# Kernel tuning notes

Hardware: AMD Instinct MI355X
Metric: run time of the kernel (lower is better)

Reference implementation:

```python
import jax, jax.numpy as jnp
import numpy as np

N = 100000   # nodes
E = 800000   # edges (avg degree 8)
D = 64       # in_feats == n_hidden
L = 3        # n_layers
BN_EPS = 1e-5


def _l2norm(h):
    # F.normalize(dim=-1), eps=1e-12
    n = jnp.linalg.norm(h, axis=-1, keepdims=True)
    return h / jnp.maximum(n, 1e-12)


def setup_inputs() -> dict:
    key = jax.random.key(0)
    ks = jax.random.split(key, 16)
    s = 0.05
    x = jax.random.uniform(ks[0], (N, D), dtype=jnp.float32) * 10.0  # count-like, nonneg
    edge_src = jax.random.randint(ks[1], (E,), 0, N, dtype=jnp.int32)
    edge_dst = jax.random.randint(ks[2], (E,), 0, N, dtype=jnp.int32)
    return {
        "x": x,
        "edge_src": edge_src,
        "edge_dst": edge_dst,
        "W_self": jax.random.normal(ks[3], (L, D, D), jnp.float32) * s,
        "W_neigh": jax.random.normal(ks[4], (L, D, D), jnp.float32) * s,
        "b_sage": jnp.zeros((L, D), jnp.float32),
        "fc_w": jax.random.normal(ks[5], (D, D), jnp.float32) * s,
        "fc_b": jnp.zeros((D,), jnp.float32),
        "bn_gamma": jnp.ones((D,), jnp.float32),
        "bn_beta": jnp.zeros((D,), jnp.float32),
        "bn_mean": jax.random.normal(ks[6], (D,), jnp.float32) * 0.1,
        "bn_var": jax.random.uniform(ks[7], (D,), jnp.float32) + 0.5,
        "fc21_w": jax.random.normal(ks[8], (D, D), jnp.float32) * s,
        "fc21_b": jnp.zeros((D,), jnp.float32),
        "fc22_w": jax.random.normal(ks[9], (D, D), jnp.float32) * s,
        "fc22_b": jnp.zeros((D,), jnp.float32),
    }


def reference(x, edge_src, edge_dst, W_self, W_neigh, b_sage, fc_w, fc_b,
              bn_gamma, bn_beta, bn_mean, bn_var, fc21_w, fc21_b, fc22_w, fc22_b):
    n = x.shape[0]
    h = jnp.log(x + 1.0)
    # mean-aggregator degree normalization (clamped at 1 like DGL)
    deg = jax.ops.segment_sum(jnp.ones(edge_dst.shape, h.dtype), edge_dst, num_segments=n)
    deg = jnp.maximum(deg, 1.0)[:, None]
    for l in range(L):
        neigh = jax.ops.segment_sum(h[edge_src], edge_dst, num_segments=n) / deg
        h = h @ W_self[l] + neigh @ W_neigh[l] + b_sage[l]
        if l < L - 1:  # last SAGEConv has no activation / norm
            h = _l2norm(jax.nn.relu(h))
    # fc head: Linear -> BatchNorm1d(eval) -> ReLU -> Softplus
    h = h @ fc_w + fc_b
    h = (h - bn_mean) * jax.lax.rsqrt(bn_var + BN_EPS) * bn_gamma + bn_beta
    h = jax.nn.relu(h)
    h = jax.nn.softplus(h)
    z_loc = h @ fc21_w + fc21_b
    z_scale = jnp.exp(h @ fc22_w + fc22_b)
    return (z_loc, z_scale)
```

## Files before the change

### kernel.cpp

```cpp
#include <hip/hip_runtime.h>
#include <math.h>

#define NN 100000
#define NE 800000
#define NB 512
#define EPB 4096

typedef short bf16x8 __attribute__((ext_vector_type(8)));
typedef float f32x4 __attribute__((ext_vector_type(4)));
typedef unsigned short u16x8 __attribute__((ext_vector_type(8)));
typedef unsigned short u16x4 __attribute__((ext_vector_type(4)));

__device__ __forceinline__ float bf2f(unsigned short u) {
    union { unsigned u32; float f; } c; c.u32 = ((unsigned)u) << 16; return c.f;
}
__device__ __forceinline__ unsigned short f2bf(float f) {
    union { float f; unsigned u; } c; c.f = f;
    unsigned u = c.u;
    unsigned r = (u + 0x7fffu + ((u >> 16) & 1u)) >> 16;
    return (unsigned short)r;
}
__device__ __forceinline__ int bucket_of(int d) {
    return (int)(((long long)d * NB) / NN);
}
__device__ __forceinline__ int node_start_of(int b) {
    return (int)(((long long)b * NN) / NB);
}


__global__ void zero_kernel(int* __restrict__ deg, int* __restrict__ gcursor) {
    int i = blockIdx.x * 256 + threadIdx.x;
    if (i < NN) deg[i] = 0;
    if (i < NB) gcursor[i] = 0;
}

__global__ void deg_kernel(const int* __restrict__ dst, int* __restrict__ deg) {
    int e = blockIdx.x * 256 + threadIdx.x;
    if (e < NE) atomicAdd(&deg[dst[e]], 1);
}

__global__ void partial_sum_kernel(const int* __restrict__ deg, int* __restrict__ partial) {
    int base = blockIdx.x * 2048 + threadIdx.x * 8;
    int s = 0;
    #pragma unroll
    for (int j = 0; j < 8; j++) { int i = base + j; if (i < NN) s += deg[i]; }
    #pragma unroll
    for (int off = 32; off > 0; off >>= 1) s += __shfl_down(s, off);
    __shared__ int ws[4];
    int lane = threadIdx.x & 63, w = threadIdx.x >> 6;
    if (lane == 0) ws[w] = s;
    __syncthreads();
    if (threadIdx.x == 0) partial[blockIdx.x] = ws[0] + ws[1] + ws[2] + ws[3];
}

__global__ void scan_partials_kernel(int* __restrict__ partial) {
    int lane = threadIdx.x;
    int v = (lane < 49) ? partial[lane] : 0;
    int s = v;
    #pragma unroll
    for (int off = 1; off < 64; off <<= 1) { int t = __shfl_up(s, off); if (lane >= off) s += t; }
    if (lane < 49) partial[lane] = s - v;
}

__global__ void scan_write_kernel(const int* __restrict__ deg, const int* __restrict__ partial,
                                  int* __restrict__ row_ptr) {
    int base = blockIdx.x * 2048 + threadIdx.x * 8;
    int v[8]; int s = 0;
    #pragma unroll
    for (int j = 0; j < 8; j++) { int i = base + j; v[j] = (i < NN) ? deg[i] : 0; s += v[j]; }
    int lane = threadIdx.x & 63, w = threadIdx.x >> 6;
    int incl = s;
    #pragma unroll
    for (int off = 1; off < 64; off <<= 1) { int t = __shfl_up(incl, off); if (lane >= off) incl += t; }
    __shared__ int ws[4];
    if (lane == 63) ws[w] = incl;
    __syncthreads();
    int woff = 0;
    for (int i = 0; i < w; i++) woff += ws[i];
    int run = partial[blockIdx.x] + woff + incl - s;
    #pragma unroll
    for (int j = 0; j < 8; j++) { int i = base + j; if (i < NN) row_ptr[i] = run; run += v[j]; }
    if (blockIdx.x == 0 && threadIdx.x == 0) row_ptr[NN] = NE;
}

__global__ void region_start_kernel(const int* __restrict__ row_ptr, int* __restrict__ region) {
    int b = blockIdx.x * 256 + threadIdx.x;
    if (b < NB) region[b] = row_ptr[node_start_of(b)];
}

__global__ __launch_bounds__(256) void bin_edges_kernel(
        const int* __restrict__ src, const int* __restrict__ dst,
        const int* __restrict__ region, int* __restrict__ gcursor,
        int* __restrict__ pairs) {
    __shared__ int hist[NB];
    __shared__ int base[NB];
    int e0 = blockIdx.x * EPB;
    int e1 = min(e0 + EPB, NE);
    for (int i = threadIdx.x; i < NB; i += 256) hist[i] = 0;
    __syncthreads();
    for (int e = e0 + threadIdx.x; e < e1; e += 256)
        atomicAdd(&hist[bucket_of(dst[e])], 1);
    __syncthreads();
    for (int i = threadIdx.x; i < NB; i += 256) {
        int c = hist[i];
        base[i] = c ? atomicAdd(&gcursor[i], c) : 0;
        hist[i] = 0;
    }
    __syncthreads();
    for (int e = e0 + threadIdx.x; e < e1; e += 256) {
        int d = dst[e];
        int b = bucket_of(d);
        int li = d - node_start_of(b);
        int r = atomicAdd(&hist[b], 1);
        unsigned idx = (unsigned)(region[b] + base[b] + r);
        if (idx < NE) pairs[idx] = (src[e] << 8) | li;
    }
}

__global__ __launch_bounds__(256) void csr_place_kernel(
        const int* __restrict__ pairs, const int* __restrict__ row_ptr,
        int* __restrict__ col) {
    int b = blockIdx.x;
    int ns = node_start_of(b);
    int cnt = node_start_of(b + 1) - ns;
    __shared__ int rp[200];
    __shared__ int cur[200];
    for (int i = threadIdx.x; i <= cnt; i += 256) rp[i] = row_ptr[ns + i];
    for (int i = threadIdx.x; i < cnt; i += 256) cur[i] = 0;
    __syncthreads();
    int eb = rp[0], ee = rp[cnt];
    for (int p = eb + threadIdx.x; p < ee; p += 256) {
        int pr = pairs[p];
        int li = pr & 255;
        if (li < cnt) {
            int pos = atomicAdd(&cur[li], 1);
            unsigned q = (unsigned)(rp[li] + pos);
            if (q < NE) col[q] = pr >> 8;
        }
    }
}


__global__ void pack_w_kernel(const float* __restrict__ Wself, const float* __restrict__ Wneigh,
                              const float* __restrict__ fcw, const float* __restrict__ w21,
                              const float* __restrict__ w22, unsigned short* __restrict__ pack) {
    int tid = blockIdx.x * 256 + threadIdx.x;
    if (tid >= 9 * 4096) return;
    int m = tid / 4096, r = tid % 4096;
    int e = r & 7, l = (r >> 3) & 63, kb = (r >> 9) & 1, nt = r >> 10;
    int k = kb * 32 + (l >> 4) * 8 + e;
    int n = nt * 16 + (l & 15);
    const float* src;
    if (m < 3) src = Wself + m * 4096;
    else if (m < 6) src = Wneigh + (m - 3) * 4096;
    else if (m == 6) src = fcw;
    else if (m == 7) src = w21;
    else src = w22;
    pack[tid] = f2bf(src[k * 64 + n]);
}


__global__ void log1p_kernel(const float* __restrict__ x, unsigned short* __restrict__ h) {
    int i = blockIdx.x * 256 + threadIdx.x;
    if (i < NN * 16) {
        float4 v = ((const float4*)x)[i];
        u16x4 o;
        o[0] = f2bf(__logf(v.x + 1.f)); o[1] = f2bf(__logf(v.y + 1.f));
        o[2] = f2bf(__logf(v.z + 1.f)); o[3] = f2bf(__logf(v.w + 1.f));
        ((u16x4*)h)[i] = o;
    }
}

__global__ __launch_bounds__(256) void aggregate_kernel(
        const unsigned short* __restrict__ h, const int* __restrict__ row_ptr,
        const int* __restrict__ col, unsigned short* __restrict__ out) {
    int gt = blockIdx.x * 256 + threadIdx.x;
    int node = gt >> 6;
    if (node >= NN) return;
    int lane = threadIdx.x & 63;
    int slot = lane >> 3;
    int f = (lane & 7) * 8;
    int beg = row_ptr[node], end = row_ptr[node + 1];
    float a0 = 0.f, a1 = 0.f, a2 = 0.f, a3 = 0.f, a4 = 0.f, a5 = 0.f, a6 = 0.f, a7 = 0.f;
    for (int p = beg + slot; p < end; p += 16) {
        int p1 = p + 8;
        unsigned s0 = min((unsigned)col[p], (unsigned)(NN - 1));
        u16x8 v0 = *(const u16x8*)(h + (size_t)s0 * 64 + f);
        if (p1 < end) {
            unsigned s1 = min((unsigned)col[p1], (unsigned)(NN - 1));
            u16x8 v1 = *(const u16x8*)(h + (size_t)s1 * 64 + f);
            a0 += bf2f(v1[0]); a1 += bf2f(v1[1]); a2 += bf2f(v1[2]); a3 += bf2f(v1[3]);
            a4 += bf2f(v1[4]); a5 += bf2f(v1[5]); a6 += bf2f(v1[6]); a7 += bf2f(v1[7]);
        }
        a0 += bf2f(v0[0]); a1 += bf2f(v0[1]); a2 += bf2f(v0[2]); a3 += bf2f(v0[3]);
        a4 += bf2f(v0[4]); a5 += bf2f(v0[5]); a6 += bf2f(v0[6]); a7 += bf2f(v0[7]);
    }
    #pragma unroll
    for (int off = 8; off < 64; off <<= 1) {
        a0 += __shfl_xor(a0, off); a1 += __shfl_xor(a1, off);
        a2 += __shfl_xor(a2, off); a3 += __shfl_xor(a3, off);
        a4 += __shfl_xor(a4, off); a5 += __shfl_xor(a5, off);
        a6 += __shfl_xor(a6, off); a7 += __shfl_xor(a7, off);
    }
    if (lane < 8) {
        float inv = 1.f / fmaxf((float)(end - beg), 1.f);
        u16x8 o;
        o[0] = f2bf(a0 * inv); o[1] = f2bf(a1 * inv); o[2] = f2bf(a2 * inv); o[3] = f2bf(a3 * inv);
        o[4] = f2bf(a4 * inv); o[5] = f2bf(a5 * inv); o[6] = f2bf(a6 * inv); o[7] = f2bf(a7 * inv);
        *(u16x8*)(out + (size_t)node * 64 + f) = o;
    }
}


template <bool ACT>
__global__ __launch_bounds__(256) void sage_mfma_kernel(
        const unsigned short* __restrict__ hin, unsigned short* __restrict__ hnb,
        const unsigned short* __restrict__ packS, const unsigned short* __restrict__ packN,
        const float* __restrict__ bias) {
    int wid = threadIdx.x >> 6, l = threadIdx.x & 63;
    int row_base = blockIdx.x * 64 + wid * 16;
    int arow = row_base + (l & 15);
    int koff = (l >> 4) * 8;
    bf16x8 z = {0, 0, 0, 0, 0, 0, 0, 0};
    bf16x8 aS0 = z, aS1 = z, aN0 = z, aN1 = z;
    if (arow < NN) {
        const unsigned short* hp = hin + (size_t)arow * 64 + koff;
        const unsigned short* np = hnb + (size_t)arow * 64 + koff;
        aS0 = *(const bf16x8*)(hp);
        aS1 = *(const bf16x8*)(hp + 32);
        aN0 = *(const bf16x8*)(np);
        aN1 = *(const bf16x8*)(np + 32);
    }
    int col0 = l & 15;
    int ro4 = (l >> 4) * 4;
    float ss0 = 0.f, ss1 = 0.f, ss2 = 0.f, ss3 = 0.f;
    f32x4 accs[4];
    #pragma unroll
    for (int nt = 0; nt < 4; nt++) {
        bf16x8 b0 = *(const bf16x8*)(packS + ((nt * 2 + 0) * 64 + l) * 8);
        bf16x8 b1 = *(const bf16x8*)(packS + ((nt * 2 + 1) * 64 + l) * 8);
        bf16x8 c0 = *(const bf16x8*)(packN + ((nt * 2 + 0) * 64 + l) * 8);
        bf16x8 c1 = *(const bf16x8*)(packN + ((nt * 2 + 1) * 64 + l) * 8);
        f32x4 acc = {0.f, 0.f, 0.f, 0.f};
        acc = __builtin_amdgcn_mfma_f32_16x16x32_bf16(aS0, b0, acc, 0, 0, 0);
        acc = __builtin_amdgcn_mfma_f32_16x16x32_bf16(aS1, b1, acc, 0, 0, 0);
        acc = __builtin_amdgcn_mfma_f32_16x16x32_bf16(aN0, c0, acc, 0, 0, 0);
        acc = __builtin_amdgcn_mfma_f32_16x16x32_bf16(aN1, c1, acc, 0, 0, 0);
        float bv = bias[nt * 16 + col0];
        #pragma unroll
        for (int j = 0; j < 4; j++) {
            float v = acc[j] + bv;
            if (ACT) {
                v = fmaxf(v, 0.f);
                if (j == 0) ss0 = fmaf(v, v, ss0);
                if (j == 1) ss1 = fmaf(v, v, ss1);
                if (j == 2) ss2 = fmaf(v, v, ss2);
                if (j == 3) ss3 = fmaf(v, v, ss3);
            }
            acc[j] = v;
        }
        accs[nt] = acc;
    }
    if (ACT) {
        #pragma unroll
        for (int off = 1; off < 16; off <<= 1) {
            ss0 += __shfl_xor(ss0, off); ss1 += __shfl_xor(ss1, off);
            ss2 += __shfl_xor(ss2, off); ss3 += __shfl_xor(ss3, off);
        }
        float i0 = 1.f / fmaxf(sqrtf(ss0), 1e-12f);
        float i1 = 1.f / fmaxf(sqrtf(ss1), 1e-12f);
        float i2 = 1.f / fmaxf(sqrtf(ss2), 1e-12f);
        float i3 = 1.f / fmaxf(sqrtf(ss3), 1e-12f);
        #pragma unroll
        for (int nt = 0; nt < 4; nt++) {
            accs[nt][0] *= i0; accs[nt][1] *= i1; accs[nt][2] *= i2; accs[nt][3] *= i3;
        }
    }
    #pragma unroll
    for (int j = 0; j < 4; j++) {
        int row = row_base + ro4 + j;
        if (row < NN) {
            #pragma unroll
            for (int nt = 0; nt < 4; nt++)
                hnb[(size_t)row * 64 + nt * 16 + col0] = f2bf(accs[nt][j]);
        }
    }
}

__global__ __launch_bounds__(256) void head_mfma_kernel(
        const unsigned short* __restrict__ h,
        const unsigned short* __restrict__ packFC, const float* __restrict__ fc_b,
        const float* __restrict__ bn_g, const float* __restrict__ bn_b,
        const float* __restrict__ bn_m, const float* __restrict__ bn_v,
        const unsigned short* __restrict__ pack21, const float* __restrict__ b21,
        const unsigned short* __restrict__ pack22, const float* __restrict__ b22,
        float* __restrict__ zloc, float* __restrict__ zscale) {
    __shared__ unsigned short tl[4][16][72];
    int wid = threadIdx.x >> 6, l = threadIdx.x & 63;
    int row_base = blockIdx.x * 64 + wid * 16;
    int arow = row_base + (l & 15);
    int koff = (l >> 4) * 8;
    bf16x8 z = {0, 0, 0, 0, 0, 0, 0, 0};
    bf16x8 a0 = z, a1 = z;
    if (arow < NN) {
        const unsigned short* hp = h + (size_t)arow * 64 + koff;
        a0 = *(const bf16x8*)(hp);
        a1 = *(const bf16x8*)(hp + 32);
    }
    int col0 = l & 15;
    int ro4 = (l >> 4) * 4;

    #pragma unroll
    for (int nt = 0; nt < 4; nt++) {
        bf16x8 b0 = *(const bf16x8*)(packFC + ((nt * 2 + 0) * 64 + l) * 8);
        bf16x8 b1 = *(const bf16x8*)(packFC + ((nt * 2 + 1) * 64 + l) * 8);
        f32x4 acc = {0.f, 0.f, 0.f, 0.f};
        acc = __builtin_amdgcn_mfma_f32_16x16x32_bf16(a0, b0, acc, 0, 0, 0);
        acc = __builtin_amdgcn_mfma_f32_16x16x32_bf16(a1, b1, acc, 0, 0, 0);
        int col = nt * 16 + col0;
        float scale = bn_g[col] * rsqrtf(bn_v[col] + 1e-5f);
        float mm = bn_m[col], bb = bn_b[col], fb = fc_b[col];
        #pragma unroll
        for (int j = 0; j < 4; j++) {
            float u = (acc[j] + fb - mm) * scale + bb;
            u = fmaxf(u, 0.f);
            float t = u + __logf(1.f + __expf(-u));
            tl[wid][ro4 + j][col] = f2bf(t);
        }
    }
    __syncthreads();
    bf16x8 t0 = *(const bf16x8*)(&tl[wid][l & 15][koff]);
    bf16x8 t1 = *(const bf16x8*)(&tl[wid][l & 15][32 + koff]);

    #pragma unroll
    for (int nt = 0; nt < 4; nt++) {
        bf16x8 b0 = *(const bf16x8*)(pack21 + ((nt * 2 + 0) * 64 + l) * 8);
        bf16x8 b1 = *(const bf16x8*)(pack21 + ((nt * 2 + 1) * 64 + l) * 8);
        f32x4 acc = {0.f, 0.f, 0.f, 0.f};
        acc = __builtin_amdgcn_mfma_f32_16x16x32_bf16(t0, b0, acc, 0, 0, 0);
        acc = __builtin_amdgcn_mfma_f32_16x16x32_bf16(t1, b1, acc, 0, 0, 0);
        int col = nt * 16 + col0;
        float bv = b21[col];
        #pragma unroll
        for (int j = 0; j < 4; j++) {
            int row = row_base + ro4 + j;
            if (row < NN) zloc[(size_t)row * 64 + col] = acc[j] + bv;
        }
    }

    #pragma unroll
    for (int nt = 0; nt < 4; nt++) {
        bf16x8 b0 = *(const bf16x8*)(pack22 + ((nt * 2 + 0) * 64 + l) * 8);
        bf16x8 b1 = *(const bf16x8*)(pack22 + ((nt * 2 + 1) * 64 + l) * 8);
        f32x4 acc = {0.f, 0.f, 0.f, 0.f};
        acc = __builtin_amdgcn_mfma_f32_16x16x32_bf16(t0, b0, acc, 0, 0, 0);
        acc = __builtin_amdgcn_mfma_f32_16x16x32_bf16(t1, b1, acc, 0, 0, 0);
        int col = nt * 16 + col0;
        float bv = b22[col];
        #pragma unroll
        for (int j = 0; j < 4; j++) {
            int row = row_base + ro4 + j;
            if (row < NN) zscale[(size_t)row * 64 + col] = __expf(acc[j] + bv);
        }
    }
}


extern "C" void kernel_launch(void* const* d_in, const int* in_sizes, int n_in,
                              void* d_out, int out_size, void* d_ws, size_t ws_size,
                              hipStream_t stream) {
    const float* x       = (const float*)d_in[0];
    const int*   esrc    = (const int*)d_in[1];
    const int*   edst    = (const int*)d_in[2];
    const float* W_self  = (const float*)d_in[3];
    const float* W_neigh = (const float*)d_in[4];
    const float* b_sage  = (const float*)d_in[5];
    const float* fc_w    = (const float*)d_in[6];
    const float* fc_b    = (const float*)d_in[7];
    const float* bn_g    = (const float*)d_in[8];
    const float* bn_b    = (const float*)d_in[9];
    const float* bn_m    = (const float*)d_in[10];
    const float* bn_v    = (const float*)d_in[11];
    const float* w21     = (const float*)d_in[12];
    const float* b21     = (const float*)d_in[13];
    const float* w22     = (const float*)d_in[14];
    const float* b22     = (const float*)d_in[15];

    float* zloc   = (float*)d_out;
    float* zscale = zloc + (size_t)NN * 64;

    unsigned short* hb0  = (unsigned short*)d_ws;
    unsigned short* hb1  = hb0 + (size_t)NN * 64;
    unsigned short* pack = hb1 + (size_t)NN * 64;
    int* pairs   = (int*)(pack + 9 * 4096);
    int* deg     = pairs + NE;
    int* row_ptr = deg + NN;
    int* col     = row_ptr + NN + 1;
    int* gcursor = col + NE;
    int* region  = gcursor + NB;
    int* partial = region + NB;

    zero_kernel<<<(NN + 255) / 256, 256, 0, stream>>>(deg, gcursor);
    deg_kernel<<<(NE + 255) / 256, 256, 0, stream>>>(edst, deg);
    partial_sum_kernel<<<49, 256, 0, stream>>>(deg, partial);
    scan_partials_kernel<<<1, 64, 0, stream>>>(partial);
    scan_write_kernel<<<49, 256, 0, stream>>>(deg, partial, row_ptr);
    region_start_kernel<<<(NB + 255) / 256, 256, 0, stream>>>(row_ptr, region);
    bin_edges_kernel<<<(NE + EPB - 1) / EPB, 256, 0, stream>>>(esrc, edst, region, gcursor, pairs);
    csr_place_kernel<<<NB, 256, 0, stream>>>(pairs, row_ptr, col);

    pack_w_kernel<<<(9 * 4096 + 255) / 256, 256, 0, stream>>>(
        W_self, W_neigh, fc_w, w21, w22, pack);
    log1p_kernel<<<(NN * 16 + 255) / 256, 256, 0, stream>>>(x, hb0);

    const int gemm_grid = (NN + 63) / 64;

    unsigned short* hc = hb0;
    unsigned short* hn = hb1;
    for (int l = 0; l < 3; l++) {
        aggregate_kernel<<<(NN * 64 + 255) / 256, 256, 0, stream>>>(hc, row_ptr, col, hn);
        unsigned short* pS = pack + l * 4096;
        unsigned short* pN = pack + (3 + l) * 4096;
        if (l < 2)
            sage_mfma_kernel<true><<<gemm_grid, 256, 0, stream>>>(
                hc, hn, pS, pN, b_sage + l * 64);
        else
            sage_mfma_kernel<false><<<gemm_grid, 256, 0, stream>>>(
                hc, hn, pS, pN, b_sage + l * 64);
        unsigned short* t = hc; hc = hn; hn = t;
    }

    head_mfma_kernel<<<gemm_grid, 256, 0, stream>>>(
        hc, pack + 6 * 4096, fc_b, bn_g, bn_b, bn_m, bn_v,
        pack + 7 * 4096, b21, pack + 8 * 4096, b22, zloc, zscale);
}
```

Before: 241.1 us.

## Fuse neighbor aggregation into SAGE MFMA kernel and streamline CSR build

Neighbor mean aggregation now runs inside the SAGE GEMM kernel. Each wave gathers its 16 rows into LDS and feeds them straight to the MFMA, which removes the separate aggregate launch and the write and re-read of the aggregated buffer in global memory. CSR construction drops the per-node degree atomics and the three-kernel prefix scan. It uses bucket-level histograms and a single-block scan, then computes per-node offsets locally inside csr_place. The catch is that each wave now walks 16 nodes one after another, one node per lane slot, so the gather has less parallelism and occupancy may suffer. The per-bucket serial scan in one thread also adds a little latency.

```diff
diff --git a/kernel.cpp b/kernel.cpp
--- a/kernel.cpp
+++ b/kernel.cpp
@@ -28,69 +28,47 @@
 }
 
 
-__global__ void zero_kernel(int* __restrict__ deg, int* __restrict__ gcursor) {
+__global__ void zero_kernel(int* __restrict__ gcount) {
     int i = blockIdx.x * 256 + threadIdx.x;
-    if (i < NN) deg[i] = 0;
-    if (i < NB) gcursor[i] = 0;
-}
-
-__global__ void deg_kernel(const int* __restrict__ dst, int* __restrict__ deg) {
-    int e = blockIdx.x * 256 + threadIdx.x;
-    if (e < NE) atomicAdd(&deg[dst[e]], 1);
-}
-
-__global__ void partial_sum_kernel(const int* __restrict__ deg, int* __restrict__ partial) {
-    int base = blockIdx.x * 2048 + threadIdx.x * 8;
-    int s = 0;
-    #pragma unroll
-    for (int j = 0; j < 8; j++) { int i = base + j; if (i < NN) s += deg[i]; }
-    #pragma unroll
-    for (int off = 32; off > 0; off >>= 1) s += __shfl_down(s, off);
-    __shared__ int ws[4];
-    int lane = threadIdx.x & 63, w = threadIdx.x >> 6;
-    if (lane == 0) ws[w] = s;
-    __syncthreads();
-    if (threadIdx.x == 0) partial[blockIdx.x] = ws[0] + ws[1] + ws[2] + ws[3];
-}
-
-__global__ void scan_partials_kernel(int* __restrict__ partial) {
-    int lane = threadIdx.x;
-    int v = (lane < 49) ? partial[lane] : 0;
-    int s = v;
-    #pragma unroll
-    for (int off = 1; off < 64; off <<= 1) { int t = __shfl_up(s, off); if (lane >= off) s += t; }
-    if (lane < 49) partial[lane] = s - v;
-}
-
-__global__ void scan_write_kernel(const int* __restrict__ deg, const int* __restrict__ partial,
-                                  int* __restrict__ row_ptr) {
-    int base = blockIdx.x * 2048 + threadIdx.x * 8;
-    int v[8]; int s = 0;
-    #pragma unroll
-    for (int j = 0; j < 8; j++) { int i = base + j; v[j] = (i < NN) ? deg[i] : 0; s += v[j]; }
-    int lane = threadIdx.x & 63, w = threadIdx.x >> 6;
-    int incl = s;
-    #pragma unroll
-    for (int off = 1; off < 64; off <<= 1) { int t = __shfl_up(incl, off); if (lane >= off) incl += t; }
-    __shared__ int ws[4];
+    if (i < NB) gcount[i] = 0;
+}
+
+__global__ __launch_bounds__(256) void bucket_hist_kernel(
+        const int* __restrict__ dst, int* __restrict__ gcount) {
+    __shared__ int hist[NB];
+    int e0 = blockIdx.x * EPB;
+    int e1 = min(e0 + EPB, NE);
+    for (int i = threadIdx.x; i < NB; i += 256) hist[i] = 0;
+    __syncthreads();
+    for (int e = e0 + threadIdx.x; e < e1; e += 256)
+        atomicAdd(&hist[bucket_of(dst[e])], 1);
+    __syncthreads();
+    for (int i = threadIdx.x; i < NB; i += 256)
+        if (hist[i]) atomicAdd(&gcount[i], hist[i]);
+}
+
+__global__ __launch_bounds__(512) void bucket_scan_kernel(
+        const int* __restrict__ gcount, int* __restrict__ bucket_base,
+        int* __restrict__ gcursor) {
+    __shared__ int ws[8];
+    int t = threadIdx.x, lane = t & 63, w = t >> 6;
+    int v = gcount[t];
+    int incl = v;
+    #pragma unroll
+    for (int off = 1; off < 64; off <<= 1) { int s = __shfl_up(incl, off); if (lane >= off) incl += s; }
     if (lane == 63) ws[w] = incl;
     __syncthreads();
     int woff = 0;
     for (int i = 0; i < w; i++) woff += ws[i];
-    int run = partial[blockIdx.x] + woff + incl - s;
-    #pragma unroll
-    for (int j = 0; j < 8; j++) { int i = base + j; if (i < NN) row_ptr[i] = run; run += v[j]; }
-    if (blockIdx.x == 0 && threadIdx.x == 0) row_ptr[NN] = NE;
-}
-
-__global__ void region_start_kernel(const int* __restrict__ row_ptr, int* __restrict__ region) {
-    int b = blockIdx.x * 256 + threadIdx.x;
-    if (b < NB) region[b] = row_ptr[node_start_of(b)];
+    int excl = woff + incl - v;
+    bucket_base[t] = excl;
+    gcursor[t] = 0;
+    if (t == NB - 1) bucket_base[NB] = excl + v;
 }
 
 __global__ __launch_bounds__(256) void bin_edges_kernel(
         const int* __restrict__ src, const int* __restrict__ dst,
-        const int* __restrict__ region, int* __restrict__ gcursor,
+        const int* __restrict__ bucket_base, int* __restrict__ gcursor,
         int* __restrict__ pairs) {
     __shared__ int hist[NB];
     __shared__ int base[NB];
@@ -112,29 +90,44 @@
         int b = bucket_of(d);
         int li = d - node_start_of(b);
         int r = atomicAdd(&hist[b], 1);
-        unsigned idx = (unsigned)(region[b] + base[b] + r);
+        unsigned idx = (unsigned)(bucket_base[b] + base[b] + r);
         if (idx < NE) pairs[idx] = (src[e] << 8) | li;
     }
 }
 
 __global__ __launch_bounds__(256) void csr_place_kernel(
-        const int* __restrict__ pairs, const int* __restrict__ row_ptr,
-        int* __restrict__ col) {
+        const int* __restrict__ pairs, const int* __restrict__ bucket_base,
+        int* __restrict__ row_ptr, int* __restrict__ col) {
     int b = blockIdx.x;
     int ns = node_start_of(b);
     int cnt = node_start_of(b + 1) - ns;
-    __shared__ int rp[200];
     __shared__ int cur[200];
-    for (int i = threadIdx.x; i <= cnt; i += 256) rp[i] = row_ptr[ns + i];
+    __shared__ int off[200];
+    int eb = bucket_base[b], ee = bucket_base[b + 1];
     for (int i = threadIdx.x; i < cnt; i += 256) cur[i] = 0;
     __syncthreads();
-    int eb = rp[0], ee = rp[cnt];
+    for (int p = eb + threadIdx.x; p < ee; p += 256) {
+        int li = pairs[p] & 255;
+        if (li < cnt) atomicAdd(&cur[li], 1);
+    }
+    __syncthreads();
+    if (threadIdx.x == 0) {
+        int run = 0;
+        for (int i = 0; i < cnt; i++) { off[i] = run; run += cur[i]; }
+    }
+    __syncthreads();
+    for (int i = threadIdx.x; i < cnt; i += 256) {
+        row_ptr[ns + i] = eb + off[i];
+        cur[i] = 0;
+    }
+    if (b == NB - 1 && threadIdx.x == 0) row_ptr[NN] = NE;
+    __syncthreads();
     for (int p = eb + threadIdx.x; p < ee; p += 256) {
         int pr = pairs[p];
         int li = pr & 255;
         if (li < cnt) {
             int pos = atomicAdd(&cur[li], 1);
-            unsigned q = (unsigned)(rp[li] + pos);
+            unsigned q = (unsigned)(eb + off[li] + pos);
             if (q < NE) col[q] = pr >> 8;
         }
     }
@@ -171,66 +164,64 @@
     }
 }
 
-__global__ __launch_bounds__(256) void aggregate_kernel(
-        const unsigned short* __restrict__ h, const int* __restrict__ row_ptr,
-        const int* __restrict__ col, unsigned short* __restrict__ out) {
-    int gt = blockIdx.x * 256 + threadIdx.x;
-    int node = gt >> 6;
-    if (node >= NN) return;
-    int lane = threadIdx.x & 63;
-    int slot = lane >> 3;
-    int f = (lane & 7) * 8;
-    int beg = row_ptr[node], end = row_ptr[node + 1];
-    float a0 = 0.f, a1 = 0.f, a2 = 0.f, a3 = 0.f, a4 = 0.f, a5 = 0.f, a6 = 0.f, a7 = 0.f;
-    for (int p = beg + slot; p < end; p += 16) {
-        int p1 = p + 8;
-        unsigned s0 = min((unsigned)col[p], (unsigned)(NN - 1));
-        u16x8 v0 = *(const u16x8*)(h + (size_t)s0 * 64 + f);
-        if (p1 < end) {
-            unsigned s1 = min((unsigned)col[p1], (unsigned)(NN - 1));
-            u16x8 v1 = *(const u16x8*)(h + (size_t)s1 * 64 + f);
-            a0 += bf2f(v1[0]); a1 += bf2f(v1[1]); a2 += bf2f(v1[2]); a3 += bf2f(v1[3]);
-            a4 += bf2f(v1[4]); a5 += bf2f(v1[5]); a6 += bf2f(v1[6]); a7 += bf2f(v1[7]);
-        }
-        a0 += bf2f(v0[0]); a1 += bf2f(v0[1]); a2 += bf2f(v0[2]); a3 += bf2f(v0[3]);
-        a4 += bf2f(v0[4]); a5 += bf2f(v0[5]); a6 += bf2f(v0[6]); a7 += bf2f(v0[7]);
-    }
-    #pragma unroll
-    for (int off = 8; off < 64; off <<= 1) {
-        a0 += __shfl_xor(a0, off); a1 += __shfl_xor(a1, off);
-        a2 += __shfl_xor(a2, off); a3 += __shfl_xor(a3, off);
-        a4 += __shfl_xor(a4, off); a5 += __shfl_xor(a5, off);
-        a6 += __shfl_xor(a6, off); a7 += __shfl_xor(a7, off);
-    }
-    if (lane < 8) {
-        float inv = 1.f / fmaxf((float)(end - beg), 1.f);
-        u16x8 o;
-        o[0] = f2bf(a0 * inv); o[1] = f2bf(a1 * inv); o[2] = f2bf(a2 * inv); o[3] = f2bf(a3 * inv);
-        o[4] = f2bf(a4 * inv); o[5] = f2bf(a5 * inv); o[6] = f2bf(a6 * inv); o[7] = f2bf(a7 * inv);
-        *(u16x8*)(out + (size_t)node * 64 + f) = o;
-    }
-}
-
 
 template <bool ACT>
-__global__ __launch_bounds__(256) void sage_mfma_kernel(
-        const unsigned short* __restrict__ hin, unsigned short* __restrict__ hnb,
+__global__ __launch_bounds__(256) void agg_sage_kernel(
+        const unsigned short* __restrict__ hc, unsigned short* __restrict__ hn,
+        const int* __restrict__ row_ptr, const int* __restrict__ col,
         const unsigned short* __restrict__ packS, const unsigned short* __restrict__ packN,
         const float* __restrict__ bias) {
+    __shared__ unsigned short tl[4][16][72];
     int wid = threadIdx.x >> 6, l = threadIdx.x & 63;
     int row_base = blockIdx.x * 64 + wid * 16;
+    int slot = l >> 3;
+    int f = (l & 7) * 8;
+
+    for (int i = 0; i < 16; i++) {
+        int node = row_base + i;
+        if (node >= NN) break;
+        int beg = row_ptr[node], end = row_ptr[node + 1];
+        float a0 = 0.f, a1 = 0.f, a2 = 0.f, a3 = 0.f, a4 = 0.f, a5 = 0.f, a6 = 0.f, a7 = 0.f;
+        for (int p = beg + slot; p < end; p += 16) {
+            int p1 = p + 8;
+            unsigned s0 = min((unsigned)col[p], (unsigned)(NN - 1));
+            u16x8 v0 = *(const u16x8*)(hc + (size_t)s0 * 64 + f);
+            if (p1 < end) {
+                unsigned s1 = min((unsigned)col[p1], (unsigned)(NN - 1));
+                u16x8 v1 = *(const u16x8*)(hc + (size_t)s1 * 64 + f);
+                a0 += bf2f(v1[0]); a1 += bf2f(v1[1]); a2 += bf2f(v1[2]); a3 += bf2f(v1[3]);
+                a4 += bf2f(v1[4]); a5 += bf2f(v1[5]); a6 += bf2f(v1[6]); a7 += bf2f(v1[7]);
+            }
+            a0 += bf2f(v0[0]); a1 += bf2f(v0[1]); a2 += bf2f(v0[2]); a3 += bf2f(v0[3]);
+            a4 += bf2f(v0[4]); a5 += bf2f(v0[5]); a6 += bf2f(v0[6]); a7 += bf2f(v0[7]);
+        }
+        #pragma unroll
+        for (int off = 8; off < 64; off <<= 1) {
+            a0 += __shfl_xor(a0, off); a1 += __shfl_xor(a1, off);
+            a2 += __shfl_xor(a2, off); a3 += __shfl_xor(a3, off);
+            a4 += __shfl_xor(a4, off); a5 += __shfl_xor(a5, off);
+            a6 += __shfl_xor(a6, off); a7 += __shfl_xor(a7, off);
+        }
+        if (l < 8) {
+            float inv = 1.f / fmaxf((float)(end - beg), 1.f);
+            u16x8 o;
+            o[0] = f2bf(a0 * inv); o[1] = f2bf(a1 * inv); o[2] = f2bf(a2 * inv); o[3] = f2bf(a3 * inv);
+            o[4] = f2bf(a4 * inv); o[5] = f2bf(a5 * inv); o[6] = f2bf(a6 * inv); o[7] = f2bf(a7 * inv);
+            *(u16x8*)(&tl[wid][i][f]) = o;
+        }
+    }
+
     int arow = row_base + (l & 15);
     int koff = (l >> 4) * 8;
     bf16x8 z = {0, 0, 0, 0, 0, 0, 0, 0};
-    bf16x8 aS0 = z, aS1 = z, aN0 = z, aN1 = z;
+    bf16x8 aS0 = z, aS1 = z;
     if (arow < NN) {
-        const unsigned short* hp = hin + (size_t)arow * 64 + koff;
-        const unsigned short* np = hnb + (size_t)arow * 64 + koff;
+        const unsigned short* hp = hc + (size_t)arow * 64 + koff;
         aS0 = *(const bf16x8*)(hp);
         aS1 = *(const bf16x8*)(hp + 32);
-        aN0 = *(const bf16x8*)(np);
-        aN1 = *(const bf16x8*)(np + 32);
-    }
+    }
+    bf16x8 aN0 = *(const bf16x8*)(&tl[wid][l & 15][koff]);
+    bf16x8 aN1 = *(const bf16x8*)(&tl[wid][l & 15][32 + koff]);
     int col0 = l & 15;
     int ro4 = (l >> 4) * 4;
     float ss0 = 0.f, ss1 = 0.f, ss2 = 0.f, ss3 = 0.f;
@@ -282,7 +273,7 @@
         if (row < NN) {
             #pragma unroll
             for (int nt = 0; nt < 4; nt++)
-                hnb[(size_t)row * 64 + nt * 16 + col0] = f2bf(accs[nt][j]);
+                hn[(size_t)row * 64 + nt * 16 + col0] = f2bf(accs[nt][j]);
         }
     }
 }
@@ -392,22 +383,19 @@
     unsigned short* hb0  = (unsigned short*)d_ws;
     unsigned short* hb1  = hb0 + (size_t)NN * 64;
     unsigned short* pack = hb1 + (size_t)NN * 64;
-    int* pairs   = (int*)(pack + 9 * 4096);
-    int* deg     = pairs + NE;
-    int* row_ptr = deg + NN;
-    int* col     = row_ptr + NN + 1;
-    int* gcursor = col + NE;
-    int* region  = gcursor + NB;
-    int* partial = region + NB;
-
-    zero_kernel<<<(NN + 255) / 256, 256, 0, stream>>>(deg, gcursor);
-    deg_kernel<<<(NE + 255) / 256, 256, 0, stream>>>(edst, deg);
-    partial_sum_kernel<<<49, 256, 0, stream>>>(deg, partial);
-    scan_partials_kernel<<<1, 64, 0, stream>>>(partial);
-    scan_write_kernel<<<49, 256, 0, stream>>>(deg, partial, row_ptr);
-    region_start_kernel<<<(NB + 255) / 256, 256, 0, stream>>>(row_ptr, region);
-    bin_edges_kernel<<<(NE + EPB - 1) / EPB, 256, 0, stream>>>(esrc, edst, region, gcursor, pairs);
-    csr_place_kernel<<<NB, 256, 0, stream>>>(pairs, row_ptr, col);
+    int* pairs       = (int*)(pack + 9 * 4096);
+    int* row_ptr     = pairs + NE;
+    int* col         = row_ptr + NN + 1;
+    int* gcount      = col + NE;
+    int* bucket_base = gcount + NB;
+    int* gcursor     = bucket_base + NB + 1;
+
+    zero_kernel<<<2, 256, 0, stream>>>(gcount);
+    bucket_hist_kernel<<<(NE + EPB - 1) / EPB, 256, 0, stream>>>(edst, gcount);
+    bucket_scan_kernel<<<1, 512, 0, stream>>>(gcount, bucket_base, gcursor);
+    bin_edges_kernel<<<(NE + EPB - 1) / EPB, 256, 0, stream>>>(
+        esrc, edst, bucket_base, gcursor, pairs);
+    csr_place_kernel<<<NB, 256, 0, stream>>>(pairs, bucket_base, row_ptr, col);
 
     pack_w_kernel<<<(9 * 4096 + 255) / 256, 256, 0, stream>>>(
         W_self, W_neigh, fc_w, w21, w22, pack);
@@ -418,15 +406,14 @@
     unsigned short* hc = hb0;
     unsigned short* hn = hb1;
     for (int l = 0; l < 3; l++) {
-        aggregate_kernel<<<(NN * 64 + 255) / 256, 256, 0, stream>>>(hc, row_ptr, col, hn);
         unsigned short* pS = pack + l * 4096;
         unsigned short* pN = pack + (3 + l) * 4096;
         if (l < 2)
-            sage_mfma_kernel<true><<<gemm_grid, 256, 0, stream>>>(
-                hc, hn, pS, pN, b_sage + l * 64);
+            agg_sage_kernel<true><<<gemm_grid, 256, 0, stream>>>(
+                hc, hn, row_ptr, col, pS, pN, b_sage + l * 64);
         else
-            sage_mfma_kernel<false><<<gemm_grid, 256, 0, stream>>>(
-                hc, hn, pS, pN, b_sage + l * 64);
+            agg_sage_kernel<false><<<gemm_grid, 256, 0, stream>>>(
+                hc, hn, row_ptr, col, pS, pN, b_sage + l * 64);
         unsigned short* t = hc; hc = hn; hn = t;
     }
 
```

Result: faster. 230.8 us (-4.3%).
